# Kernel optimization log

Hardware: AMD Instinct MI355X
Metric: run time of the kernel (lower is better)

The kernel has to match this reference:

```python
import jax, jax.numpy as jnp
import numpy as np


def setup_inputs() -> dict:
    key = jax.random.key(0)
    k0, k1, k2, k3 = jax.random.split(key, 4)
    B, L, D, H = 8, 4096, 300, 128  # batch, leaves (power of 2), embed dim, hidden
    x = jax.random.normal(k0, (B, L, D), jnp.float32)
    W_leaf = jax.random.normal(k1, (D, 2 * H), jnp.float32) * (1.0 / np.sqrt(D))
    b_leaf = jnp.zeros((2 * H,), jnp.float32)
    W_l = jax.random.normal(k2, (H, 5 * H), jnp.float32) * (1.0 / np.sqrt(H))
    W_r = jax.random.normal(k3, (H, 5 * H), jnp.float32) * (1.0 / np.sqrt(H))
    b = jnp.zeros((5 * H,), jnp.float32)
    return {"x": x, "W_leaf": W_leaf, "b_leaf": b_leaf, "W_l": W_l, "W_r": W_r, "b": b}


def reference(x, W_leaf, b_leaf, W_l, W_r, b):
    """Binary TreeLSTM over a complete tree: leaves -> root.

    x: [B, L, D] leaf embeddings, L a power of 2.
    Leaf transform: linear projection split into (h, c) (SPINN-style).
    REDUCE: 5-gate child-sum-of-two composition.
    Returns root hidden state: [B, H].
    """
    H = W_l.shape[0]
    hc = x @ W_leaf + b_leaf                     # [B, L, 2H]
    h, c = hc[..., :H], hc[..., H:]
    levels = int(np.log2(x.shape[1]))
    for _ in range(levels):                      # level-batched tree reduction
        h_l, h_r = h[:, 0::2], h[:, 1::2]        # [B, n/2, H]
        c_l, c_r = c[:, 0::2], c[:, 1::2]
        gates = h_l @ W_l + h_r @ W_r + b        # [B, n/2, 5H]
        i, fl, fr, o, g = jnp.split(gates, 5, axis=-1)
        c = (jax.nn.sigmoid(fl) * c_l
             + jax.nn.sigmoid(fr) * c_r
             + jax.nn.sigmoid(i) * jnp.tanh(g))
        h = jax.nn.sigmoid(o) * jnp.tanh(c)
    return h[:, 0]                               # root hidden state [B, H]
```

## Files before the change

kernel.cpp:

```cpp
#include <hip/hip_runtime.h>
#include <hip/hip_bf16.h>
#include <math.h>


typedef __attribute__((ext_vector_type(8))) short bfrag8;
typedef __attribute__((ext_vector_type(4))) float f32x4;

__device__ __forceinline__ float rcpf(float x) { return __builtin_amdgcn_rcpf(x); }
__device__ __forceinline__ float sigf(float x) { return rcpf(1.0f + __expf(-x)); }
__device__ __forceinline__ float tanh_f(float x) {
    float e = __expf(2.0f * x);
    return 1.0f - 2.0f * rcpf(e + 1.0f);
}
__device__ __forceinline__ short f2bf(float f) {
    __hip_bfloat16 h = __float2bfloat16(f);
    return *reinterpret_cast<short*>(&h);
}
__device__ __forceinline__ float bf2f(short s) {
    union { unsigned int u; float f; } v;
    v.u = ((unsigned int)(unsigned short)s) << 16;
    return v.f;
}
__device__ __forceinline__ bfrag8 pack8(f32x4 a, f32x4 b) {
    union { int i[4]; bfrag8 v; } u;
    asm("v_cvt_pk_bf16_f32 %0, %1, %2" : "=v"(u.i[0]) : "v"(a[0]), "v"(a[1]));
    asm("v_cvt_pk_bf16_f32 %0, %1, %2" : "=v"(u.i[1]) : "v"(a[2]), "v"(a[3]));
    asm("v_cvt_pk_bf16_f32 %0, %1, %2" : "=v"(u.i[2]) : "v"(b[0]), "v"(b[1]));
    asm("v_cvt_pk_bf16_f32 %0, %1, %2" : "=v"(u.i[3]) : "v"(b[2]), "v"(b[3]));
    return u.v;
}
#define GLDS(gp, lp) __builtin_amdgcn_global_load_lds( \
    (const __attribute__((address_space(1))) void*)(gp), \
    (__attribute__((address_space(3))) void*)(lp), 16, 0, 0)

__global__ __launch_bounds__(256) void reorder_kernel(
    const float* __restrict__ W_l, const float* __restrict__ W_r,
    const float* __restrict__ W_leaf,
    short* __restrict__ Wcat_ch, short* __restrict__ Wleaf_ch)
{
    int idx = blockIdx.x * 256 + threadIdx.x;
    if (idx < 163840) {
        int n = idx >> 8, k = idx & 255;
        float v = (k < 128) ? W_l[k * 640 + n] : W_r[(k - 128) * 640 + n];
        Wcat_ch[(((size_t)(k >> 3)) * 640 + n) * 8 + (k & 7)] = f2bf(v);
        return;
    }
    idx -= 163840;
    if (idx < 81920) {
        int n = idx / 320, k = idx - n * 320;
        short v = (k < 300) ? f2bf(W_leaf[k * 256 + n]) : (short)0;
        Wleaf_ch[(((size_t)(k >> 3)) * 256 + n) * 8 + (k & 7)] = v;
    }
}

__global__ __launch_bounds__(256) void leaf_kernel(
    const float* __restrict__ x,   const short* __restrict__ Bw,
    const float* __restrict__ bleaf,
    short* __restrict__ hD,
    short* __restrict__ cDb)
{
    __shared__ float Als[64 * 64];
    __shared__ short Bls[8 * 256 * 8];
    const int tid  = threadIdx.x;
    const int w    = tid >> 6, lane = tid & 63;
    const int quad = lane >> 4, l16 = lane & 15;
    const int mBlk = blockIdx.x * 64;
    const int waveN = w * 64;

    f32x4 acc[4][4] = {};
    const f32x4 zero4 = {0.f, 0.f, 0.f, 0.f};

    for (int c = 0; c < 5; ++c) {
        const int k0c = c * 64;
        {
            const int q_lds = lane & 15;
            const int rsub  = lane >> 4;
            #pragma unroll
            for (int g = 0; g < 4; ++g) {
                int row = w * 16 + g * 4 + rsub;
                int q_g = (q_lds & 8) | ((q_lds & 7) ^ (row & 7));
                if (c < 4 || q_g < 11) {
                    GLDS(x + (size_t)(mBlk + row) * 300 + k0c + q_g * 4,
                         (char*)Als + (w * 16 + g * 4) * 256);
                } else {
                    *(f32x4*)((char*)Als + row * 256 + q_lds * 16) = zero4;
                }
            }
        }
        #pragma unroll
        for (int g = 0; g < 8; ++g) {
            int i   = w * 8 + g;
            int cc  = i >> 2, colg = (i & 3) * 64;
            GLDS(Bw + ((size_t)(c * 8 + cc) * 256 + colg + lane) * 8,
                 (char*)Bls + ((cc * 256 + colg)) * 16);
        }
        __syncthreads();
        #pragma unroll
        for (int ks = 0; ks < 2; ++ks) {
            const int ca = ks * 4 + quad;
            bfrag8 af[4], bf4[4];
            #pragma unroll
            for (int i = 0; i < 4; ++i) {
                int r  = i * 16 + l16;
                int u0 = 2 * ca, u1 = 2 * ca + 1;
                int s0 = (u0 & 8) | ((u0 & 7) ^ (r & 7));
                int s1 = (u1 & 8) | ((u1 & 7) ^ (r & 7));
                f32x4 a0 = *(const f32x4*)(Als + r * 64 + s0 * 4);
                f32x4 a1 = *(const f32x4*)(Als + r * 64 + s1 * 4);
                af[i] = pack8(a0, a1);
            }
            #pragma unroll
            for (int jn = 0; jn < 4; ++jn)
                bf4[jn] = *(const bfrag8*)(Bls + (ca * 256 + waveN + jn * 16 + l16) * 8);
            #pragma unroll
            for (int i = 0; i < 4; ++i)
                #pragma unroll
                for (int jn = 0; jn < 4; ++jn)
                    acc[i][jn] = __builtin_amdgcn_mfma_f32_16x16x32_bf16(
                                     af[i], bf4[jn], acc[i][jn], 0, 0, 0);
        }
        __syncthreads();
    }

    #pragma unroll
    for (int i = 0; i < 4; ++i) {
        int row0 = mBlk + i * 16 + quad * 4;
        #pragma unroll
        for (int jn = 0; jn < 4; ++jn) {
            int col = waveN + jn * 16 + l16;
            float bv = bleaf[col];
            #pragma unroll
            for (int rg = 0; rg < 4; ++rg) {
                float v = acc[i][jn][rg] + bv;
                int m = row0 + rg;
                if (col < 128) {
                    int hc = col;
                    hD[(((size_t)((m & 1) * 16 + (hc >> 3))) * 16384 + (m >> 1)) * 8
                       + (hc & 7)] = f2bf(v);
                } else {
                    int ch = col - 128;
                    cDb[(size_t)(ch >> 4) * 32768 * 16 + (size_t)m * 16 + (ch & 15)]
                        = f2bf(v);
                }
            }
        }
    }
}

template<int CIN_BF, int COUT_BF>
__global__ __launch_bounds__(256, 2) void level_ws_t(
    const short* __restrict__ A,
    const void*  __restrict__ cprev,
    const short* __restrict__ Wch,
    const float* __restrict__ bias,
    short* __restrict__ hout, void* __restrict__ cout_,
    int M, int nst)
{
    __shared__ short Als[32 * 64 * 8];
    const int tid  = threadIdx.x;
    const int w    = tid >> 6, lane = tid & 63;
    const int quad = lane >> 4, l16 = lane & 15;
    const int j   = blockIdx.y;
    const int tb0 = blockIdx.x * 64 * nst;
    const int h   = j * 16 + l16;

    #pragma unroll
    for (int s = 0; s < 8; ++s)
        GLDS(A + ((size_t)(s * 4 + w) * M + tb0 + lane) * 8,
             (char*)Als + (s * 4 + w) * 1024);

    bfrag8 Wfr[5][8];
    #pragma unroll
    for (int g = 0; g < 5; ++g)
        #pragma unroll
        for (int s = 0; s < 8; ++s)
            Wfr[g][s] = *(const bfrag8*)(Wch + ((size_t)(s * 4 + quad) * 640
                                                + g * 128 + h) * 8);
    const float bi  = bias[h],       bfl = bias[128 + h], bfr_ = bias[256 + h];
    const float bo  = bias[384 + h], bg  = bias[512 + h];

    const int Mn = M >> 1;
    for (int st = 0; st < nst; ++st) {
        const int tb = tb0 + st * 64;
        __syncthreads();

        f32x4 acc[5] = {};
        #pragma unroll
        for (int s = 0; s < 8; ++s) {
            bfrag8 af = *(const bfrag8*)(Als + ((s * 4 + quad) * 64 + w * 16 + l16) * 8);
            #pragma unroll
            for (int g = 0; g < 5; ++g)
                acc[g] = __builtin_amdgcn_mfma_f32_16x16x32_bf16(af, Wfr[g][s], acc[g], 0, 0, 0);
        }

        if (st + 1 < nst) {
            __syncthreads();
            #pragma unroll
            for (int s = 0; s < 8; ++s)
                GLDS(A + ((size_t)(s * 4 + w) * M + tb + 64 + lane) * 8,
                     (char*)Als + (s * 4 + w) * 1024);
        }

        #pragma unroll
        for (int rg = 0; rg < 4; ++rg) {
            int m = tb + w * 16 + quad * 4 + rg;
            float gi  = acc[0][rg] + bi;
            float gfl = acc[1][rg] + bfl;
            float gfr = acc[2][rg] + bfr_;
            float go  = acc[3][rg] + bo;
            float gg  = acc[4][rg] + bg;
            float cl, cr;
            if (CIN_BF) {
                const short* cp = (const short*)cprev;
                size_t base = (size_t)(h >> 4) * ((size_t)2 * M) * 16
                              + (size_t)(2 * m) * 16 + (h & 15);
                cl = bf2f(cp[base]);
                cr = bf2f(cp[base + 16]);
            } else {
                const float* cp = (const float*)cprev;
                cl = cp[(size_t)(2 * m) * 128 + h];
                cr = cp[(size_t)(2 * m + 1) * 128 + h];
            }
            float cn  = sigf(gfl) * cl + sigf(gfr) * cr + sigf(gi) * tanh_f(gg);
            float hn  = sigf(go) * tanh_f(cn);
            hout[(((size_t)((m & 1) * 16 + (h >> 3))) * Mn + (m >> 1)) * 8
                 + (h & 7)] = f2bf(hn);
            if (COUT_BF) {
                ((short*)cout_)[(size_t)(h >> 4) * (size_t)M * 16
                                + (size_t)m * 16 + (h & 15)] = f2bf(cn);
            } else {
                ((float*)cout_)[(size_t)m * 128 + h] = cn;
            }
        }
    }
}

__global__ __launch_bounds__(512) void finish_kernel(
    const short* __restrict__ hin,
    const float* __restrict__ cin,
    const short* __restrict__ Wch, const float* __restrict__ bias,
    float* __restrict__ out)
{
    __shared__ short hP[32 * 64 * 8];
    __shared__ short hQ[32 * 32 * 8];
    __shared__ float cA[128 * 128];
    __shared__ float cB[64 * 128];
    const int tid  = threadIdx.x;
    const int w    = tid >> 6, lane = tid & 63;
    const int quad = lane >> 4, l16 = lane & 15;
    const int h    = w * 16 + l16;

    #pragma unroll
    for (int g = 0; g < 4; ++g)
        GLDS(hin + ((size_t)((g * 8 + w) * 64 + lane)) * 8,
             (char*)hP + ((g * 8 + w) * 64) * 16);
    #pragma unroll
    for (int g = 0; g < 8; ++g)
        GLDS(cin + ((size_t)((g * 8 + w) * 64 + lane)) * 4,
             (char*)cA + ((g * 8 + w) * 64) * 16);

    bfrag8 Wfr[5][8];
    #pragma unroll
    for (int g = 0; g < 5; ++g)
        #pragma unroll
        for (int s = 0; s < 8; ++s)
            Wfr[g][s] = *(const bfrag8*)(Wch + ((size_t)(s * 4 + quad) * 640
                                                + g * 128 + h) * 8);
    const float bi  = bias[h],       bfl = bias[128 + h], bfr_ = bias[256 + h];
    const float bo  = bias[384 + h], bg  = bias[512 + h];

    __syncthreads();

    #pragma unroll
    for (int t = 0; t < 4; ++t) {
        const int Mo = 64 >> t;
        const short* hsrc = (t & 1) ? hQ : hP;
        short* hdst       = (t & 1) ? hP : hQ;
        const float* cread  = (t & 1) ? cB : cA;
        float*       cwrite = (t & 1) ? cA : cB;
        const int nrt = (Mo + 15) >> 4;

        for (int rt = 0; rt < nrt; ++rt) {
            f32x4 acc[5] = {};
            #pragma unroll
            for (int s = 0; s < 8; ++s) {
                bfrag8 af = *(const bfrag8*)(hsrc + ((s * 4 + quad) * Mo
                                                     + rt * 16 + l16) * 8);
                #pragma unroll
                for (int g = 0; g < 5; ++g)
                    acc[g] = __builtin_amdgcn_mfma_f32_16x16x32_bf16(
                                 af, Wfr[g][s], acc[g], 0, 0, 0);
            }
            #pragma unroll
            for (int rg = 0; rg < 4; ++rg) {
                int m = rt * 16 + quad * 4 + rg;
                if (m < Mo) {
                    float gi  = acc[0][rg] + bi;
                    float gfl = acc[1][rg] + bfl;
                    float gfr = acc[2][rg] + bfr_;
                    float go  = acc[3][rg] + bo;
                    float gg  = acc[4][rg] + bg;
                    float cl  = cread[(2 * m) * 128 + h];
                    float cr  = cread[(2 * m + 1) * 128 + h];
                    float cn  = sigf(gfl) * cl + sigf(gfr) * cr + sigf(gi) * tanh_f(gg);
                    float hn  = sigf(go) * tanh_f(cn);
                    if (t == 3) {
                        out[(size_t)m * 128 + h] = hn;
                    } else {
                        hdst[(((m & 1) * 16 + (h >> 3)) * (Mo >> 1) + (m >> 1)) * 8
                             + (h & 7)] = f2bf(hn);
                        cwrite[m * 128 + h] = cn;
                    }
                }
            }
        }
        __syncthreads();
    }
}

extern "C" void kernel_launch(void* const* d_in, const int* in_sizes, int n_in,
                              void* d_out, int out_size, void* d_ws, size_t ws_size,
                              hipStream_t stream)
{
    const float* x      = (const float*)d_in[0];
    const float* W_leaf = (const float*)d_in[1];
    const float* b_leaf = (const float*)d_in[2];
    const float* W_l    = (const float*)d_in[3];
    const float* W_r    = (const float*)d_in[4];
    const float* b      = (const float*)d_in[5];
    float* out = (float*)d_out;

    char* p = (char*)d_ws;
    short* hA    = (short*)p; p += (size_t)32 * 16384 * 16 + 1024;
    short* hB    = (short*)p; p += (size_t)32 * 8192 * 16 + 1024;
    char*  c0    = p;         p += (size_t)32768 * 128 * 4;
    char*  c1    = p;         p += (size_t)16384 * 128 * 4;
    short* WcatC = (short*)p; p += (size_t)32 * 640 * 16;
    short* WlfC  = (short*)p; p += (size_t)40 * 256 * 16;

    reorder_kernel<<<960, 256, 0, stream>>>(W_l, W_r, W_leaf, WcatC, WlfC);

    leaf_kernel<<<512, 256, 0, stream>>>(x, WlfC, b_leaf, hA, (short*)c0);

    level_ws_t<1, 1><<<dim3(16384 / 256, 8), 256, 0, stream>>>(
        hA, c0, WcatC, b, hB, c1, 16384, 4);
    level_ws_t<1, 0><<<dim3(8192 / 128, 8), 256, 0, stream>>>(
        hB, c1, WcatC, b, hA, c0, 8192, 2);

    const short* hin = hA; const char* cin = c0;
    int M = 4096;
    for (int lev = 3; lev <= 8; ++lev) {
        short* ho = (lev & 1) ? hB : hA;
        char*  co = (lev & 1) ? c1 : c0;
        int nst = (lev == 3) ? 2 : 1;
        level_ws_t<0, 0><<<dim3(M / (64 * nst), 8), 256, 0, stream>>>(
            hin, cin, WcatC, b, ho, co, M, nst);
        hin = ho; cin = co;
        M >>= 1;
    }

    finish_kernel<<<1, 512, 0, stream>>>(hA, (const float*)c0, WcatC, b, out);
}
```

Baseline: 166.2 us.

## Split leaf projection into bf16 conversion pass and weight-stationary MFMA kernel

Replaces the fused leaf GEMM, which read fp32 x and converted it to bf16 inside the MMA loop, with two kernels. The first converts x to a padded, chunk-major bf16 layout. The second keeps the weight fragments in registers per 64-column slice and streams A tiles through LDS. The intent is to cut per-tile conversion and weight reloads, at the cost of an extra launch and an extra round trip of x through global memory.

```diff
diff --git a/kernel.cpp b/kernel.cpp
--- a/kernel.cpp
+++ b/kernel.cpp
@@ -5,6 +5,7 @@
 
 typedef __attribute__((ext_vector_type(8))) short bfrag8;
 typedef __attribute__((ext_vector_type(4))) float f32x4;
+typedef __attribute__((ext_vector_type(4))) short s16x4;
 
 __device__ __forceinline__ float rcpf(float x) { return __builtin_amdgcn_rcpf(x); }
 __device__ __forceinline__ float sigf(float x) { return rcpf(1.0f + __expf(-x)); }
@@ -20,14 +21,6 @@
     union { unsigned int u; float f; } v;
     v.u = ((unsigned int)(unsigned short)s) << 16;
     return v.f;
-}
-__device__ __forceinline__ bfrag8 pack8(f32x4 a, f32x4 b) {
-    union { int i[4]; bfrag8 v; } u;
-    asm("v_cvt_pk_bf16_f32 %0, %1, %2" : "=v"(u.i[0]) : "v"(a[0]), "v"(a[1]));
-    asm("v_cvt_pk_bf16_f32 %0, %1, %2" : "=v"(u.i[1]) : "v"(a[2]), "v"(a[3]));
-    asm("v_cvt_pk_bf16_f32 %0, %1, %2" : "=v"(u.i[2]) : "v"(b[0]), "v"(b[1]));
-    asm("v_cvt_pk_bf16_f32 %0, %1, %2" : "=v"(u.i[3]) : "v"(b[2]), "v"(b[3]));
-    return u.v;
 }
 #define GLDS(gp, lp) __builtin_amdgcn_global_load_lds( \
     (const __attribute__((address_space(1))) void*)(gp), \
@@ -53,95 +46,87 @@
     }
 }
 
-__global__ __launch_bounds__(256) void leaf_kernel(
-    const float* __restrict__ x,   const short* __restrict__ Bw,
+__global__ __launch_bounds__(256) void convx_kernel(
+    const float* __restrict__ x, short* __restrict__ xbf)
+{
+    __shared__ short Ls[64 * 328];
+    const int tid = threadIdx.x;
+    const int R0 = blockIdx.x * 64;
+    for (int i = tid; i < 64 * 75; i += 256) {
+        int r = i / 75, q = i - r * 75;
+        f32x4 v = *(const f32x4*)(x + (size_t)(R0 + r) * 300 + q * 4);
+        s16x4 o;
+        #pragma unroll
+        for (int t = 0; t < 4; ++t) o[t] = f2bf(v[t]);
+        *(s16x4*)(Ls + r * 328 + q * 4) = o;
+    }
+    for (int i = tid; i < 64 * 20; i += 256) {
+        int r = i / 20, q = i - r * 20;
+        Ls[r * 328 + 300 + q] = 0;
+    }
+    __syncthreads();
+    for (int i = tid; i < 40 * 64; i += 256) {
+        int c = i >> 6, r = i & 63;
+        bfrag8 v = *(const bfrag8*)(Ls + r * 328 + c * 8);
+        *(bfrag8*)(xbf + ((size_t)c * 32768 + R0 + r) * 8) = v;
+    }
+}
+
+__global__ __launch_bounds__(256, 2) void leafws_kernel(
+    const short* __restrict__ A,
+    const short* __restrict__ Bw,
     const float* __restrict__ bleaf,
     short* __restrict__ hD,
     short* __restrict__ cDb)
 {
-    __shared__ float Als[64 * 64];
-    __shared__ short Bls[8 * 256 * 8];
+    __shared__ short Als[40 * 64 * 8];
     const int tid  = threadIdx.x;
     const int w    = tid >> 6, lane = tid & 63;
     const int quad = lane >> 4, l16 = lane & 15;
-    const int mBlk = blockIdx.x * 64;
-    const int waveN = w * 64;
-
-    f32x4 acc[4][4] = {};
-    const f32x4 zero4 = {0.f, 0.f, 0.f, 0.f};
-
-    for (int c = 0; c < 5; ++c) {
-        const int k0c = c * 64;
-        {
-            const int q_lds = lane & 15;
-            const int rsub  = lane >> 4;
-            #pragma unroll
-            for (int g = 0; g < 4; ++g) {
-                int row = w * 16 + g * 4 + rsub;
-                int q_g = (q_lds & 8) | ((q_lds & 7) ^ (row & 7));
-                if (c < 4 || q_g < 11) {
-                    GLDS(x + (size_t)(mBlk + row) * 300 + k0c + q_g * 4,
-                         (char*)Als + (w * 16 + g * 4) * 256);
-                } else {
-                    *(f32x4*)((char*)Als + row * 256 + q_lds * 16) = zero4;
-                }
-            }
-        }
-        #pragma unroll
-        for (int g = 0; g < 8; ++g) {
-            int i   = w * 8 + g;
-            int cc  = i >> 2, colg = (i & 3) * 64;
-            GLDS(Bw + ((size_t)(c * 8 + cc) * 256 + colg + lane) * 8,
-                 (char*)Bls + ((cc * 256 + colg)) * 16);
-        }
-        __syncthreads();
-        #pragma unroll
-        for (int ks = 0; ks < 2; ++ks) {
-            const int ca = ks * 4 + quad;
-            bfrag8 af[4], bf4[4];
-            #pragma unroll
-            for (int i = 0; i < 4; ++i) {
-                int r  = i * 16 + l16;
-                int u0 = 2 * ca, u1 = 2 * ca + 1;
-                int s0 = (u0 & 8) | ((u0 & 7) ^ (r & 7));
-                int s1 = (u1 & 8) | ((u1 & 7) ^ (r & 7));
-                f32x4 a0 = *(const f32x4*)(Als + r * 64 + s0 * 4);
-                f32x4 a1 = *(const f32x4*)(Als + r * 64 + s1 * 4);
-                af[i] = pack8(a0, a1);
-            }
-            #pragma unroll
-            for (int jn = 0; jn < 4; ++jn)
-                bf4[jn] = *(const bfrag8*)(Bls + (ca * 256 + waveN + jn * 16 + l16) * 8);
-            #pragma unroll
-            for (int i = 0; i < 4; ++i)
-                #pragma unroll
-                for (int jn = 0; jn < 4; ++jn)
-                    acc[i][jn] = __builtin_amdgcn_mfma_f32_16x16x32_bf16(
-                                     af[i], bf4[jn], acc[i][jn], 0, 0, 0);
-        }
-        __syncthreads();
-    }
-
-    #pragma unroll
-    for (int i = 0; i < 4; ++i) {
-        int row0 = mBlk + i * 16 + quad * 4;
-        #pragma unroll
-        for (int jn = 0; jn < 4; ++jn) {
-            int col = waveN + jn * 16 + l16;
-            float bv = bleaf[col];
-            #pragma unroll
-            for (int rg = 0; rg < 4; ++rg) {
-                float v = acc[i][jn][rg] + bv;
-                int m = row0 + rg;
-                if (col < 128) {
-                    int hc = col;
-                    hD[(((size_t)((m & 1) * 16 + (hc >> 3))) * 16384 + (m >> 1)) * 8
-                       + (hc & 7)] = f2bf(v);
-                } else {
-                    int ch = col - 128;
-                    cDb[(size_t)(ch >> 4) * 32768 * 16 + (size_t)m * 16 + (ch & 15)]
-                        = f2bf(v);
-                }
+    const int j    = blockIdx.y;
+    const int tb   = blockIdx.x * 64;
+
+    #pragma unroll
+    for (int t = 0; t < 10; ++t)
+        GLDS(A + ((size_t)(t * 4 + w) * 32768 + tb + lane) * 8,
+             (char*)Als + (t * 4 + w) * 1024);
+
+    bfrag8 Wfr[4][10];
+    #pragma unroll
+    for (int g = 0; g < 4; ++g)
+        #pragma unroll
+        for (int s = 0; s < 10; ++s)
+            Wfr[g][s] = *(const bfrag8*)(Bw + ((size_t)(s * 4 + quad) * 256
+                                               + j * 64 + g * 16 + l16) * 8);
+    float bv[4];
+    #pragma unroll
+    for (int g = 0; g < 4; ++g) bv[g] = bleaf[j * 64 + g * 16 + l16];
+
+    __syncthreads();
+
+    f32x4 acc[4] = {};
+    #pragma unroll
+    for (int s = 0; s < 10; ++s) {
+        bfrag8 af = *(const bfrag8*)(Als + ((s * 4 + quad) * 64 + w * 16 + l16) * 8);
+        #pragma unroll
+        for (int g = 0; g < 4; ++g)
+            acc[g] = __builtin_amdgcn_mfma_f32_16x16x32_bf16(af, Wfr[g][s], acc[g], 0, 0, 0);
+    }
+
+    #pragma unroll
+    for (int g = 0; g < 4; ++g) {
+        int col = j * 64 + g * 16 + l16;
+        #pragma unroll
+        for (int rg = 0; rg < 4; ++rg) {
+            int m = tb + w * 16 + quad * 4 + rg;
+            float v = acc[g][rg] + bv[g];
+            if (col < 128) {
+                hD[(((size_t)((m & 1) * 16 + (col >> 3))) * 16384 + (m >> 1)) * 8
+                   + (col & 7)] = f2bf(v);
+            } else {
+                int ch = col - 128;
+                cDb[(size_t)(ch >> 4) * 32768 * 16 + (size_t)m * 16 + (ch & 15)]
+                    = f2bf(v);
             }
         }
     }
@@ -331,6 +316,7 @@
     float* out = (float*)d_out;
 
     char* p = (char*)d_ws;
+    short* xbf   = (short*)p; p += (size_t)40 * 32768 * 16;
     short* hA    = (short*)p; p += (size_t)32 * 16384 * 16 + 1024;
     short* hB    = (short*)p; p += (size_t)32 * 8192 * 16 + 1024;
     char*  c0    = p;         p += (size_t)32768 * 128 * 4;
@@ -339,8 +325,9 @@
     short* WlfC  = (short*)p; p += (size_t)40 * 256 * 16;
 
     reorder_kernel<<<960, 256, 0, stream>>>(W_l, W_r, W_leaf, WcatC, WlfC);
-
-    leaf_kernel<<<512, 256, 0, stream>>>(x, WlfC, b_leaf, hA, (short*)c0);
+    convx_kernel<<<512, 256, 0, stream>>>(x, xbf);
+    leafws_kernel<<<dim3(512, 4), 256, 0, stream>>>(
+        xbf, WlfC, b_leaf, hA, (short*)c0);
 
     level_ws_t<1, 1><<<dim3(16384 / 256, 8), 256, 0, stream>>>(
         hA, c0, WcatC, b, hB, c1, 16384, 4);
```

After: 192.0 us. 15.5% more time.
